# Kernel optimization log

Hardware: AMD Instinct MI355X
Metric: run time of the kernel (lower is better)

## Reference

```python
import jax, jax.numpy as jnp
import numpy as np

N = 10000        # total_node
IN_SIZE = 128
OUT_SIZE = 128


def setup_inputs() -> dict:
    key = jax.random.key(0)
    k_adj, k_x, k_wn, k_ws = jax.random.split(key, 4)
    adj = jax.random.uniform(k_adj, (N, N), dtype=jnp.float32)           # package[1]
    old_node_embedding = jax.random.normal(k_x, (N, IN_SIZE), dtype=jnp.float32)
    # nn.Linear weights are stored [out, in]
    W_nei = jax.random.normal(k_wn, (OUT_SIZE, IN_SIZE), dtype=jnp.float32) * (1.0 / np.sqrt(IN_SIZE))
    W_self = jax.random.normal(k_ws, (OUT_SIZE, IN_SIZE), dtype=jnp.float32) * (1.0 / np.sqrt(IN_SIZE))
    return {
        "adj": adj,
        "old_node_embedding": old_node_embedding,
        "W_nei": W_nei,
        "W_self": W_self,
        "out_size": OUT_SIZE,
        "use_divce": 0,
    }


def reference(adj, old_node_embedding, W_nei, W_self, out_size, use_divce):
    # Vectorized form of the per-node torch loop:
    #   nei_gather[n]   = adj[n, :] @ X                (torch.mm per node)
    #   nei_info[n]     = nei_gather[n] @ W_nei^T      (nei_update1)
    #   self_info[n]    = X[n] @ W_self^T              (self_node_update1)
    #   new_emb[n]      = act(nei_info[n] + self_info[n])
    # active_method fixed to tanh.
    nei_gather = adj @ old_node_embedding                         # [N, in]
    nei_info = nei_gather @ W_nei.T                               # [N, out]
    self_info = old_node_embedding @ W_self.T                     # [N, out]
    return jnp.tanh(nei_info + self_info)
```

## Files before the change

### kernel.cpp

```cpp
#include <hip/hip_runtime.h>
#include <cmath>


#define N_NODES 10000
#define EMB 128
#define XNT_STRIDE 10240
#define KC 832
#define NKCH 13

typedef __bf16 bf16x8 __attribute__((ext_vector_type(8)));
typedef float  f32x4  __attribute__((ext_vector_type(4)));

#define GLOAD_LDS16(gp, lp)                                                  \
    __builtin_amdgcn_global_load_lds(                                        \
        (const __attribute__((address_space(1))) void*)(gp),                 \
        (__attribute__((address_space(3))) void*)(lp), 16, 0, 0)

__device__ __forceinline__ void split8(const float4& x0, const float4& x1,
                                       bf16x8& h, bf16x8& l) {
    float f[8] = {x0.x, x0.y, x0.z, x0.w, x1.x, x1.y, x1.z, x1.w};
#pragma unroll
    for (int i = 0; i < 8; ++i) {
        __bf16 hh = (__bf16)f[i];
        h[i] = hh;
        l[i] = (__bf16)(f[i] - (float)hh);
    }
}

__global__ __launch_bounds__(256) void prep_kernel(
    const float* __restrict__ X, const float* __restrict__ Wn,
    __bf16* __restrict__ xnt_hi, __bf16* __restrict__ xnt_lo)
{
    __shared__ float Xl[32 * EMB];
    const int tid = threadIdx.x;
    const int n0 = blockIdx.x * 32;

    if (blockIdx.x == 0) {
        bf16x8 z;
#pragma unroll
        for (int i = 0; i < 8; ++i) z[i] = (__bf16)0.0f;
        for (int g = tid; g < 128 * 30; g += 256) {
            int col = g / 30, j = g % 30;
            size_t off = (size_t)col * XNT_STRIDE + N_NODES + j * 8;
            *(bf16x8*)(xnt_hi + off) = z;
            *(bf16x8*)(xnt_lo + off) = z;
        }
    }

#pragma unroll
    for (int i = 0; i < 4; ++i) {
        int idx = tid + i * 256;
        int r = idx >> 5;
        int c4 = (idx & 31) << 2;
        int row = n0 + r;
        float4 v = make_float4(0.f, 0.f, 0.f, 0.f);
        if (row < N_NODES) v = *(const float4*)(X + (size_t)row * EMB + c4);
        *(float4*)(Xl + r * EMB + c4) = v;
    }
    __syncthreads();

    const int c = tid & 127;
    const int half = tid >> 7;
    const float* wrow = Wn + c * EMB;

    float acc[16];
#pragma unroll
    for (int r = 0; r < 16; ++r) acc[r] = 0.f;

    for (int k4 = 0; k4 < 32; ++k4) {
        float4 w = *(const float4*)(wrow + k4 * 4);
#pragma unroll
        for (int r = 0; r < 16; ++r) {
            float4 x = *(const float4*)(Xl + (half * 16 + r) * EMB + k4 * 4);
            acc[r] += x.x * w.x + x.y * w.y + x.z * w.z + x.w * w.w;
        }
    }

    if (n0 + half * 16 < N_NODES) {
        bf16x8 h0, h1, l0, l1;
#pragma unroll
        for (int r = 0; r < 16; ++r) {
            float f = acc[r];
            __bf16 h = (__bf16)f;
            __bf16 l = (__bf16)(f - (float)h);
            if (r < 8) { h0[r] = h; l0[r] = l; }
            else       { h1[r - 8] = h; l1[r - 8] = l; }
        }
        size_t base = (size_t)c * XNT_STRIDE + n0 + half * 16;
        *(bf16x8*)(xnt_hi + base)     = h0;
        *(bf16x8*)(xnt_hi + base + 8) = h1;
        *(bf16x8*)(xnt_lo + base)     = l0;
        *(bf16x8*)(xnt_lo + base + 8) = l1;
    }
}

__global__ __launch_bounds__(256, 2) void gemm_kernel(
    const float* __restrict__ adj, const __bf16* __restrict__ xnt_hi,
    const __bf16* __restrict__ xnt_lo, float* __restrict__ Ppart)
{
    __shared__ float  Af [128 * 64];
    __shared__ __bf16 Bhs[128 * 64];
    __shared__ __bf16 Bls[128 * 64];

    const int tid = threadIdx.x;
    const int m0 = blockIdx.x * 128;
    const int kc0 = blockIdx.y * KC;
    const int kc_end = min(kc0 + KC, N_NODES);
    const int nsub = (kc_end - kc0 + 63) >> 6;

    const int lane = tid & 63;
    const int wave = tid >> 6;
    const int wm = (wave & 1) * 64;
    const int wn = (wave >> 1) * 64;
    const int fr = lane & 15;
    const int q  = lane >> 4;
    const int f7 = fr & 7;

    const int a_c4 = ((tid & 15) ^ ((tid >> 4) & 7)) * 4;
    size_t a_rowoff[8];
#pragma unroll
    for (int i = 0; i < 8; ++i) {
        int r = i * 16 + (tid >> 4);
        if (m0 + r >= N_NODES) r &= 15;
        a_rowoff[i] = (size_t)(m0 + r) * N_NODES;
    }
    const int b_k8 = ((tid & 7) ^ ((tid >> 3) & 7)) * 8;
    size_t b_coloff[4];
#pragma unroll
    for (int i = 0; i < 4; ++i)
        b_coloff[i] = (size_t)(i * 32 + (tid >> 3)) * XNT_STRIDE;

    f32x4 acc[4][4];
#pragma unroll
    for (int mt = 0; mt < 4; ++mt)
#pragma unroll
        for (int nt = 0; nt < 4; ++nt)
#pragma unroll
            for (int e = 0; e < 4; ++e) acc[mt][nt][e] = 0.f;

    for (int ks = 0; ks < nsub; ++ks) {
        const int k0 = kc0 + ks * 64;

#pragma unroll
        for (int i = 0; i < 8; ++i) {
            int kk = k0 + a_c4;
            if (kk + 4 > kc_end) kk = kc0;
            GLOAD_LDS16(adj + a_rowoff[i] + kk, Af + (i * 256 + tid) * 4);
        }
#pragma unroll
        for (int i = 0; i < 4; ++i) {
            GLOAD_LDS16(xnt_hi + b_coloff[i] + k0 + b_k8,
                        Bhs + (i * 256 + tid) * 8);
            GLOAD_LDS16(xnt_lo + b_coloff[i] + k0 + b_k8,
                        Bls + (i * 256 + tid) * 8);
        }
        __syncthreads();

#pragma unroll
        for (int sub = 0; sub < 2; ++sub) {
            bf16x8 ah[4], al[4], bh[4], bl[4];
#pragma unroll
            for (int mt = 0; mt < 4; ++mt) {
                int r = wm + mt * 16 + fr;
                int c0 = sub * 8 + q * 2;
                int pc0 = c0 ^ f7;
                int pc1 = (c0 + 1) ^ f7;
                float4 fa = *(const float4*)(Af + r * 64 + pc0 * 4);
                float4 fb = *(const float4*)(Af + r * 64 + pc1 * 4);
                split8(fa, fb, ah[mt], al[mt]);
            }
#pragma unroll
            for (int nt = 0; nt < 4; ++nt) {
                int col = wn + nt * 16 + fr;
                int pq = (sub * 4 + q) ^ f7;
                bh[nt] = *(const bf16x8*)(Bhs + col * 64 + pq * 8);
                bl[nt] = *(const bf16x8*)(Bls + col * 64 + pq * 8);
            }
#pragma unroll
            for (int mt = 0; mt < 4; ++mt)
#pragma unroll
                for (int nt = 0; nt < 4; ++nt) {
                    acc[mt][nt] = __builtin_amdgcn_mfma_f32_16x16x32_bf16(ah[mt], bh[nt], acc[mt][nt], 0, 0, 0);
                    acc[mt][nt] = __builtin_amdgcn_mfma_f32_16x16x32_bf16(ah[mt], bl[nt], acc[mt][nt], 0, 0, 0);
                    acc[mt][nt] = __builtin_amdgcn_mfma_f32_16x16x32_bf16(al[mt], bh[nt], acc[mt][nt], 0, 0, 0);
                }
        }
        __syncthreads();
    }

    float* P = Ppart + (size_t)blockIdx.y * ((size_t)N_NODES * EMB);
#pragma unroll
    for (int mt = 0; mt < 4; ++mt) {
        int rbase = m0 + wm + mt * 16 + q * 4;
#pragma unroll
        for (int nt = 0; nt < 4; ++nt) {
            int col = wn + nt * 16 + fr;
#pragma unroll
            for (int r = 0; r < 4; ++r) {
                int row = rbase + r;
                if (row < N_NODES)
                    P[(size_t)row * EMB + col] = acc[mt][nt][r];
            }
        }
    }
}

__global__ __launch_bounds__(256) void epi_kernel(
    const float* __restrict__ X, const float* __restrict__ Wself,
    const float* __restrict__ Ppart, float* __restrict__ out)
{
    __shared__ float Xl[32 * EMB];
    const int tid = threadIdx.x;
    const int n0 = blockIdx.x * 32;

#pragma unroll
    for (int i = 0; i < 4; ++i) {
        int idx = tid + i * 256;
        int r = idx >> 5;
        int c4 = (idx & 31) << 2;
        int row = n0 + r;
        float4 v = make_float4(0.f, 0.f, 0.f, 0.f);
        if (row < N_NODES) v = *(const float4*)(X + (size_t)row * EMB + c4);
        *(float4*)(Xl + r * EMB + c4) = v;
    }
    __syncthreads();

    const int c = tid & 127;
    const int half = tid >> 7;
    const float* wrow = Wself + c * EMB;

    float acc[16];
#pragma unroll
    for (int r = 0; r < 16; ++r) acc[r] = 0.f;

    for (int k4 = 0; k4 < 32; ++k4) {
        float4 w = *(const float4*)(wrow + k4 * 4);
#pragma unroll
        for (int r = 0; r < 16; ++r) {
            float4 x = *(const float4*)(Xl + (half * 16 + r) * EMB + k4 * 4);
            acc[r] += x.x * w.x + x.y * w.y + x.z * w.z + x.w * w.w;
        }
    }

    if (n0 + half * 16 < N_NODES) {
        const size_t rb = (size_t)(n0 + half * 16) * EMB + c;
#pragma unroll
        for (int p = 0; p < NKCH; ++p) {
            const float* Pp = Ppart + (size_t)p * ((size_t)N_NODES * EMB) + rb;
#pragma unroll
            for (int r = 0; r < 16; ++r)
                acc[r] += Pp[(size_t)r * EMB];
        }
#pragma unroll
        for (int r = 0; r < 16; ++r)
            out[rb + (size_t)r * EMB] = tanhf(acc[r]);
    }
}

__global__ __launch_bounds__(256) void gemm0_kernel(
    const float* __restrict__ adj, const float* __restrict__ X,
    float* __restrict__ Y)
{
    __shared__ float As[128 * 33];
    __shared__ float Xs[32 * 132];
    const int tid = threadIdx.x;
    const int m0 = blockIdx.x * 128;
    const int kc0 = blockIdx.y * KC;
    const int kc_end = min(kc0 + KC, N_NODES);
    const int nsub = (kc_end - kc0 + 31) >> 5;

    const int am = tid >> 1, akq = tid & 1;
    const bool arv = (m0 + am) < N_NODES;
    const float* arow_p = adj + (size_t)(m0 + am) * N_NODES;
    const int xr = tid >> 3, xq = tid & 7;
    const int mq = tid >> 4, nq = tid & 15;

    float acc[8][8];
#pragma unroll
    for (int i = 0; i < 8; ++i)
#pragma unroll
        for (int j = 0; j < 8; ++j) acc[i][j] = 0.f;

    for (int ks = 0; ks < nsub; ++ks) {
        int k0 = kc0 + ks * 32;
#pragma unroll
        for (int i = 0; i < 4; ++i) {
            int k = k0 + akq * 16 + i * 4;
            float4 v = make_float4(0.f, 0.f, 0.f, 0.f);
            if (arv && k < kc_end) v = *(const float4*)(arow_p + k);
            float* d = As + am * 33 + akq * 16 + i * 4;
            d[0] = v.x; d[1] = v.y; d[2] = v.z; d[3] = v.w;
        }
#pragma unroll
        for (int i = 0; i < 4; ++i) {
            int c0 = xq * 16 + i * 4;
            int krow = k0 + xr;
            float4 v = make_float4(0.f, 0.f, 0.f, 0.f);
            if (krow < kc_end) v = *(const float4*)(X + (size_t)krow * EMB + c0);
            *(float4*)(Xs + xr * 132 + c0) = v;
        }
        __syncthreads();
        for (int k = 0; k < 32; ++k) {
            float a8[8];
#pragma unroll
            for (int i = 0; i < 8; ++i) a8[i] = As[(mq * 8 + i) * 33 + k];
            float4 x0 = *(const float4*)(Xs + k * 132 + nq * 8);
            float4 x1 = *(const float4*)(Xs + k * 132 + nq * 8 + 4);
            float x8[8] = { x0.x, x0.y, x0.z, x0.w, x1.x, x1.y, x1.z, x1.w };
#pragma unroll
            for (int i = 0; i < 8; ++i)
#pragma unroll
                for (int j = 0; j < 8; ++j) acc[i][j] += a8[i] * x8[j];
        }
        __syncthreads();
    }
#pragma unroll
    for (int i = 0; i < 8; ++i) {
        int row = m0 + mq * 8 + i;
        if (row < N_NODES) {
#pragma unroll
            for (int j = 0; j < 8; ++j)
                atomicAdd(Y + (size_t)row * EMB + nq * 8 + j, acc[i][j]);
        }
    }
}

__global__ __launch_bounds__(256) void epi0_kernel(
    const float* __restrict__ X, const float* __restrict__ Wn,
    const float* __restrict__ Ws, float* __restrict__ out)
{
    __shared__ float Xl[32 * EMB];
    __shared__ float Yl[32 * EMB];
    const int tid = threadIdx.x;
    const int n0 = blockIdx.x * 32;

#pragma unroll
    for (int i = 0; i < 4; ++i) {
        int idx = tid + i * 256;
        int r = idx >> 5;
        int c4 = (idx & 31) << 2;
        int row = n0 + r;
        float4 vx = make_float4(0.f, 0.f, 0.f, 0.f);
        float4 vy = vx;
        if (row < N_NODES) {
            vx = *(const float4*)(X + (size_t)row * EMB + c4);
            vy = *(const float4*)(out + (size_t)row * EMB + c4);
        }
        *(float4*)(Xl + r * EMB + c4) = vx;
        *(float4*)(Yl + r * EMB + c4) = vy;
    }
    __syncthreads();

    const int c = tid & 127;
    const int half = tid >> 7;
    const float* wn = Wn + c * EMB;
    const float* ws = Ws + c * EMB;

    float accn[16], accs[16];
#pragma unroll
    for (int r = 0; r < 16; ++r) { accn[r] = 0.f; accs[r] = 0.f; }

    for (int k4 = 0; k4 < 32; ++k4) {
        float4 a = *(const float4*)(wn + k4 * 4);
        float4 b = *(const float4*)(ws + k4 * 4);
#pragma unroll
        for (int r = 0; r < 16; ++r) {
            float4 y = *(const float4*)(Yl + (half * 16 + r) * EMB + k4 * 4);
            float4 x = *(const float4*)(Xl + (half * 16 + r) * EMB + k4 * 4);
            accn[r] += y.x * a.x + y.y * a.y + y.z * a.z + y.w * a.w;
            accs[r] += x.x * b.x + x.y * b.y + x.z * b.z + x.w * b.w;
        }
    }
#pragma unroll
    for (int r = 0; r < 16; ++r) {
        int row = n0 + half * 16 + r;
        if (row < N_NODES)
            out[(size_t)row * EMB + c] = tanhf(accn[r] + accs[r]);
    }
}

extern "C" void kernel_launch(void* const* d_in, const int* in_sizes, int n_in,
                              void* d_out, int out_size, void* d_ws, size_t ws_size,
                              hipStream_t stream) {
    const float* adj = (const float*)d_in[0];
    const float* X   = (const float*)d_in[1];
    const float* Wn  = (const float*)d_in[2];
    const float* Ws  = (const float*)d_in[3];
    float* out = (float*)d_out;

    const size_t xnt_elems = (size_t)EMB * XNT_STRIDE;
    const size_t xnt_bytes = xnt_elems * 2 * sizeof(unsigned short);
    const size_t part_bytes = (size_t)NKCH * N_NODES * EMB * sizeof(float);

    if (ws_size >= xnt_bytes + part_bytes) {
        __bf16* xh = (__bf16*)d_ws;
        __bf16* xl = xh + xnt_elems;
        float* Ppart = (float*)((char*)d_ws + xnt_bytes);
        prep_kernel<<<(N_NODES + 31) / 32, 256, 0, stream>>>(X, Wn, xh, xl);
        gemm_kernel<<<dim3((N_NODES + 127) / 128, NKCH), 256, 0, stream>>>(adj, xh, xl, Ppart);
        epi_kernel<<<(N_NODES + 31) / 32, 256, 0, stream>>>(X, Ws, Ppart, out);
    } else {
        hipMemsetAsync(d_out, 0, (size_t)N_NODES * EMB * sizeof(float), stream);
        gemm0_kernel<<<dim3((N_NODES + 127) / 128, NKCH), 256, 0, stream>>>(adj, X, out);
        epi0_kernel<<<(N_NODES + 31) / 32, 256, 0, stream>>>(X, Wn, Ws, out);
    }
}
```

Before: 606.7 us.

## Fuse epilogue into GEMM via last-block split-K reduction and precompute self term

The self-linear term X@Ws^T is now computed in the prep kernel alongside X@Wn^T and stored to a buffer. The separate epilogue kernel is removed. Instead, each GEMM block atomically increments a per-row-strip counter, and the last K-chunk block to finish reduces all partial sums plus the self term, then applies tanh. This saves one kernel launch and the redundant X reload, at the cost of serialising the reduction onto one block per strip and adding atomics and fences.

After: 685.0 us. 1.13x slower.

```diff
diff --git a/kernel.cpp b/kernel.cpp
--- a/kernel.cpp
+++ b/kernel.cpp
@@ -7,6 +7,7 @@
 #define XNT_STRIDE 10240
 #define KC 832
 #define NKCH 13
+#define NSTRIP 79
 
 typedef __bf16 bf16x8 __attribute__((ext_vector_type(8)));
 typedef float  f32x4  __attribute__((ext_vector_type(4)));
@@ -29,7 +30,9 @@
 
 __global__ __launch_bounds__(256) void prep_kernel(
     const float* __restrict__ X, const float* __restrict__ Wn,
-    __bf16* __restrict__ xnt_hi, __bf16* __restrict__ xnt_lo)
+    const float* __restrict__ Ws,
+    __bf16* __restrict__ xnt_hi, __bf16* __restrict__ xnt_lo,
+    float* __restrict__ Sbuf, int* __restrict__ cnt)
 {
     __shared__ float Xl[32 * EMB];
     const int tid = threadIdx.x;
@@ -45,6 +48,7 @@
             *(bf16x8*)(xnt_hi + off) = z;
             *(bf16x8*)(xnt_lo + off) = z;
         }
+        for (int i = tid; i < NSTRIP; i += 256) cnt[i] = 0;
     }
 
 #pragma unroll
@@ -61,18 +65,21 @@
 
     const int c = tid & 127;
     const int half = tid >> 7;
-    const float* wrow = Wn + c * EMB;
-
-    float acc[16];
-#pragma unroll
-    for (int r = 0; r < 16; ++r) acc[r] = 0.f;
+    const float* wnrow = Wn + c * EMB;
+    const float* wsrow = Ws + c * EMB;
+
+    float accn[16], accs[16];
+#pragma unroll
+    for (int r = 0; r < 16; ++r) { accn[r] = 0.f; accs[r] = 0.f; }
 
     for (int k4 = 0; k4 < 32; ++k4) {
-        float4 w = *(const float4*)(wrow + k4 * 4);
+        float4 a = *(const float4*)(wnrow + k4 * 4);
+        float4 b = *(const float4*)(wsrow + k4 * 4);
 #pragma unroll
         for (int r = 0; r < 16; ++r) {
             float4 x = *(const float4*)(Xl + (half * 16 + r) * EMB + k4 * 4);
-            acc[r] += x.x * w.x + x.y * w.y + x.z * w.z + x.w * w.w;
+            accn[r] += x.x * a.x + x.y * a.y + x.z * a.z + x.w * a.w;
+            accs[r] += x.x * b.x + x.y * b.y + x.z * b.z + x.w * b.w;
         }
     }
 
@@ -80,7 +87,7 @@
         bf16x8 h0, h1, l0, l1;
 #pragma unroll
         for (int r = 0; r < 16; ++r) {
-            float f = acc[r];
+            float f = accn[r];
             __bf16 h = (__bf16)f;
             __bf16 l = (__bf16)(f - (float)h);
             if (r < 8) { h0[r] = h; l0[r] = l; }
@@ -91,16 +98,23 @@
         *(bf16x8*)(xnt_hi + base + 8) = h1;
         *(bf16x8*)(xnt_lo + base)     = l0;
         *(bf16x8*)(xnt_lo + base + 8) = l1;
+        size_t sb = (size_t)(n0 + half * 16) * EMB + c;
+#pragma unroll
+        for (int r = 0; r < 16; ++r)
+            Sbuf[sb + (size_t)r * EMB] = accs[r];
     }
 }
 
 __global__ __launch_bounds__(256, 2) void gemm_kernel(
     const float* __restrict__ adj, const __bf16* __restrict__ xnt_hi,
-    const __bf16* __restrict__ xnt_lo, float* __restrict__ Ppart)
+    const __bf16* __restrict__ xnt_lo, float* __restrict__ Ppart,
+    const float* __restrict__ Sbuf, int* __restrict__ cnt,
+    float* __restrict__ out)
 {
     __shared__ float  Af [128 * 64];
     __shared__ __bf16 Bhs[128 * 64];
     __shared__ __bf16 Bls[128 * 64];
+    __shared__ int s_last;
 
     const int tid = threadIdx.x;
     const int m0 = blockIdx.x * 128;
@@ -203,57 +217,40 @@
             }
         }
     }
-}
-
-__global__ __launch_bounds__(256) void epi_kernel(
-    const float* __restrict__ X, const float* __restrict__ Wself,
-    const float* __restrict__ Ppart, float* __restrict__ out)
-{
-    __shared__ float Xl[32 * EMB];
-    const int tid = threadIdx.x;
-    const int n0 = blockIdx.x * 32;
-
-#pragma unroll
-    for (int i = 0; i < 4; ++i) {
-        int idx = tid + i * 256;
-        int r = idx >> 5;
-        int c4 = (idx & 31) << 2;
-        int row = n0 + r;
-        float4 v = make_float4(0.f, 0.f, 0.f, 0.f);
-        if (row < N_NODES) v = *(const float4*)(X + (size_t)row * EMB + c4);
-        *(float4*)(Xl + r * EMB + c4) = v;
-    }
+
     __syncthreads();
-
-    const int c = tid & 127;
-    const int half = tid >> 7;
-    const float* wrow = Wself + c * EMB;
-
-    float acc[16];
-#pragma unroll
-    for (int r = 0; r < 16; ++r) acc[r] = 0.f;
-
-    for (int k4 = 0; k4 < 32; ++k4) {
-        float4 w = *(const float4*)(wrow + k4 * 4);
+    if (tid == 0) {
+        __threadfence();
+        s_last = (atomicAdd(cnt + blockIdx.x, 1) == NKCH - 1) ? 1 : 0;
+    }
+    __syncthreads();
+    if (!s_last) return;
+    __threadfence();
+
+    const int c4 = (tid & 31) * 4;
+    const int g  = tid >> 5;
+    const int rb = m0 + g * 16;
+    if (rb >= N_NODES) return;
+    const size_t off = (size_t)rb * EMB + c4;
+
+    f32x4 v[16];
+#pragma unroll
+    for (int r = 0; r < 16; ++r)
+        v[r] = *(const f32x4*)(Sbuf + off + (size_t)r * EMB);
+    for (int p = 0; p < NKCH; ++p) {
+        const float* Pp = Ppart + (size_t)p * ((size_t)N_NODES * EMB) + off;
 #pragma unroll
         for (int r = 0; r < 16; ++r) {
-            float4 x = *(const float4*)(Xl + (half * 16 + r) * EMB + k4 * 4);
-            acc[r] += x.x * w.x + x.y * w.y + x.z * w.z + x.w * w.w;
-        }
-    }
-
-    if (n0 + half * 16 < N_NODES) {
-        const size_t rb = (size_t)(n0 + half * 16) * EMB + c;
-#pragma unroll
-        for (int p = 0; p < NKCH; ++p) {
-            const float* Pp = Ppart + (size_t)p * ((size_t)N_NODES * EMB) + rb;
-#pragma unroll
-            for (int r = 0; r < 16; ++r)
-                acc[r] += Pp[(size_t)r * EMB];
-        }
-#pragma unroll
-        for (int r = 0; r < 16; ++r)
-            out[rb + (size_t)r * EMB] = tanhf(acc[r]);
+            f32x4 qv = *(const f32x4*)(Pp + (size_t)r * EMB);
+            v[r] += qv;
+        }
+    }
+#pragma unroll
+    for (int r = 0; r < 16; ++r) {
+        f32x4 t;
+#pragma unroll
+        for (int e = 0; e < 4; ++e) t[e] = tanhf(v[r][e]);
+        *(f32x4*)(out + off + (size_t)r * EMB) = t;
     }
 }
 
@@ -390,15 +387,19 @@
 
     const size_t xnt_elems = (size_t)EMB * XNT_STRIDE;
     const size_t xnt_bytes = xnt_elems * 2 * sizeof(unsigned short);
-    const size_t part_bytes = (size_t)NKCH * N_NODES * EMB * sizeof(float);
-
-    if (ws_size >= xnt_bytes + part_bytes) {
+    const size_t part_elems = (size_t)NKCH * N_NODES * EMB;
+    const size_t part_bytes = part_elems * sizeof(float);
+    const size_t s_elems = (size_t)N_NODES * EMB;
+    const size_t s_bytes = s_elems * sizeof(float);
+
+    if (ws_size >= xnt_bytes + part_bytes + s_bytes + 1024) {
         __bf16* xh = (__bf16*)d_ws;
         __bf16* xl = xh + xnt_elems;
         float* Ppart = (float*)((char*)d_ws + xnt_bytes);
-        prep_kernel<<<(N_NODES + 31) / 32, 256, 0, stream>>>(X, Wn, xh, xl);
-        gemm_kernel<<<dim3((N_NODES + 127) / 128, NKCH), 256, 0, stream>>>(adj, xh, xl, Ppart);
-        epi_kernel<<<(N_NODES + 31) / 32, 256, 0, stream>>>(X, Ws, Ppart, out);
+        float* Sbuf  = Ppart + part_elems;
+        int*   cnt   = (int*)(Sbuf + s_elems);
+        prep_kernel<<<(N_NODES + 31) / 32, 256, 0, stream>>>(X, Wn, Ws, xh, xl, Sbuf, cnt);
+        gemm_kernel<<<dim3(NSTRIP, NKCH), 256, 0, stream>>>(adj, xh, xl, Ppart, Sbuf, cnt, out);
     } else {
         hipMemsetAsync(d_out, 0, (size_t)N_NODES * EMB * sizeof(float), stream);
         gemm0_kernel<<<dim3((N_NODES + 127) / 128, NKCH), 256, 0, stream>>>(adj, X, out);
```

## Double-buffer GEMM LDS tiles with K-step 32 to overlap loads and MFMA

Applied to the files above, without the earlier changes.

Splits the shared-memory tiles for adj and the hi/lo bf16 X^T into two buffers of half the K depth (32 instead of 64). The next tile's global-to-LDS load is issued before computing on the current one, so memory latency can overlap with MFMA work, and one barrier per step is removed. Total LDS stays the same, but each step does half as much compute per sync, and the swizzle patterns were changed to match the new 32-wide rows. There is a risk of LDS bank conflicts or too little latency hiding at the shallower depth.

New measurement: 604.7 us. About the same (-0.3%).

```diff
diff --git a/kernel.cpp b/kernel.cpp
--- a/kernel.cpp
+++ b/kernel.cpp
@@ -98,15 +98,15 @@
     const float* __restrict__ adj, const __bf16* __restrict__ xnt_hi,
     const __bf16* __restrict__ xnt_lo, float* __restrict__ Ppart)
 {
-    __shared__ float  Af [128 * 64];
-    __shared__ __bf16 Bhs[128 * 64];
-    __shared__ __bf16 Bls[128 * 64];
+    __shared__ float  Af [2][128 * 32];
+    __shared__ __bf16 Bhs[2][128 * 32];
+    __shared__ __bf16 Bls[2][128 * 32];
 
     const int tid = threadIdx.x;
     const int m0 = blockIdx.x * 128;
     const int kc0 = blockIdx.y * KC;
     const int kc_end = min(kc0 + KC, N_NODES);
-    const int nsub = (kc_end - kc0 + 63) >> 6;
+    const int nsub = (kc_end - kc0 + 31) >> 5;
 
     const int lane = tid & 63;
     const int wave = tid >> 6;
@@ -116,19 +116,19 @@
     const int q  = lane >> 4;
     const int f7 = fr & 7;
 
-    const int a_c4 = ((tid & 15) ^ ((tid >> 4) & 7)) * 4;
-    size_t a_rowoff[8];
-#pragma unroll
-    for (int i = 0; i < 8; ++i) {
-        int r = i * 16 + (tid >> 4);
+    const int a_c4 = ((tid & 7) ^ ((tid >> 3) & 7)) * 4;
+    size_t a_rowoff[4];
+#pragma unroll
+    for (int i = 0; i < 4; ++i) {
+        int r = i * 32 + (tid >> 3);
         if (m0 + r >= N_NODES) r &= 15;
         a_rowoff[i] = (size_t)(m0 + r) * N_NODES;
     }
-    const int b_k8 = ((tid & 7) ^ ((tid >> 3) & 7)) * 8;
-    size_t b_coloff[4];
-#pragma unroll
-    for (int i = 0; i < 4; ++i)
-        b_coloff[i] = (size_t)(i * 32 + (tid >> 3)) * XNT_STRIDE;
+    const int b_k8 = ((tid & 3) ^ ((tid >> 3) & 3)) * 8;
+    size_t b_coloff[2];
+#pragma unroll
+    for (int i = 0; i < 2; ++i)
+        b_coloff[i] = (size_t)(i * 64 + (tid >> 2)) * XNT_STRIDE;
 
     f32x4 acc[4][4];
 #pragma unroll
@@ -138,53 +138,61 @@
 #pragma unroll
             for (int e = 0; e < 4; ++e) acc[mt][nt][e] = 0.f;
 
-    for (int ks = 0; ks < nsub; ++ks) {
-        const int k0 = kc0 + ks * 64;
-
-#pragma unroll
-        for (int i = 0; i < 8; ++i) {
+    auto stage = [&](int ks, int pb) {
+        const int k0 = kc0 + ks * 32;
+#pragma unroll
+        for (int i = 0; i < 4; ++i) {
             int kk = k0 + a_c4;
             if (kk + 4 > kc_end) kk = kc0;
-            GLOAD_LDS16(adj + a_rowoff[i] + kk, Af + (i * 256 + tid) * 4);
-        }
-#pragma unroll
-        for (int i = 0; i < 4; ++i) {
+            GLOAD_LDS16(adj + a_rowoff[i] + kk, &Af[pb][(i * 256 + tid) * 4]);
+        }
+#pragma unroll
+        for (int i = 0; i < 2; ++i) {
             GLOAD_LDS16(xnt_hi + b_coloff[i] + k0 + b_k8,
-                        Bhs + (i * 256 + tid) * 8);
+                        &Bhs[pb][(i * 256 + tid) * 8]);
             GLOAD_LDS16(xnt_lo + b_coloff[i] + k0 + b_k8,
-                        Bls + (i * 256 + tid) * 8);
-        }
-        __syncthreads();
-
-#pragma unroll
-        for (int sub = 0; sub < 2; ++sub) {
-            bf16x8 ah[4], al[4], bh[4], bl[4];
-#pragma unroll
-            for (int mt = 0; mt < 4; ++mt) {
-                int r = wm + mt * 16 + fr;
-                int c0 = sub * 8 + q * 2;
-                int pc0 = c0 ^ f7;
-                int pc1 = (c0 + 1) ^ f7;
-                float4 fa = *(const float4*)(Af + r * 64 + pc0 * 4);
-                float4 fb = *(const float4*)(Af + r * 64 + pc1 * 4);
-                split8(fa, fb, ah[mt], al[mt]);
+                        &Bls[pb][(i * 256 + tid) * 8]);
+        }
+    };
+
+    stage(0, 0);
+    __syncthreads();
+
+    for (int ks = 0; ks < nsub; ++ks) {
+        const int cb = ks & 1;
+        if (ks + 1 < nsub) stage(ks + 1, cb ^ 1);
+
+        const float*  af  = &Af [cb][0];
+        const __bf16* bhp = &Bhs[cb][0];
+        const __bf16* blp = &Bls[cb][0];
+
+        bf16x8 ah[4], al[4], bh[4], bl[4];
+#pragma unroll
+        for (int mt = 0; mt < 4; ++mt) {
+            int r = wm + mt * 16 + fr;
+            int c0 = q * 2;
+            int pc0 = c0 ^ f7;
+            int pc1 = (c0 + 1) ^ f7;
+            float4 fa = *(const float4*)(af + r * 32 + pc0 * 4);
+            float4 fb = *(const float4*)(af + r * 32 + pc1 * 4);
+            split8(fa, fb, ah[mt], al[mt]);
+        }
+#pragma unroll
+        for (int nt = 0; nt < 4; ++nt) {
+            int col = wn + nt * 16 + fr;
+            int pq = q ^ ((fr >> 1) & 3);
+            bh[nt] = *(const bf16x8*)(bhp + col * 32 + pq * 8);
+            bl[nt] = *(const bf16x8*)(blp + col * 32 + pq * 8);
+        }
+#pragma unroll
+        for (int mt = 0; mt < 4; ++mt)
+#pragma unroll
+            for (int nt = 0; nt < 4; ++nt) {
+                acc[mt][nt] = __builtin_amdgcn_mfma_f32_16x16x32_bf16(ah[mt], bh[nt], acc[mt][nt], 0, 0, 0);
+                acc[mt][nt] = __builtin_amdgcn_mfma_f32_16x16x32_bf16(ah[mt], bl[nt], acc[mt][nt], 0, 0, 0);
+                acc[mt][nt] = __builtin_amdgcn_mfma_f32_16x16x32_bf16(al[mt], bh[nt], acc[mt][nt], 0, 0, 0);
             }
-#pragma unroll
-            for (int nt = 0; nt < 4; ++nt) {
-                int col = wn + nt * 16 + fr;
-                int pq = (sub * 4 + q) ^ f7;
-                bh[nt] = *(const bf16x8*)(Bhs + col * 64 + pq * 8);
-                bl[nt] = *(const bf16x8*)(Bls + col * 64 + pq * 8);
-            }
-#pragma unroll
-            for (int mt = 0; mt < 4; ++mt)
-#pragma unroll
-                for (int nt = 0; nt < 4; ++nt) {
-                    acc[mt][nt] = __builtin_amdgcn_mfma_f32_16x16x32_bf16(ah[mt], bh[nt], acc[mt][nt], 0, 0, 0);
-                    acc[mt][nt] = __builtin_amdgcn_mfma_f32_16x16x32_bf16(ah[mt], bl[nt], acc[mt][nt], 0, 0, 0);
-                    acc[mt][nt] = __builtin_amdgcn_mfma_f32_16x16x32_bf16(al[mt], bh[nt], acc[mt][nt], 0, 0, 0);
-                }
-        }
+
         __syncthreads();
     }
 
```
